# Performance work log

Hardware: AMD Instinct MI355X
Metric: run time of the kernel (lower is better)

Reference implementation:

```python
import jax, jax.numpy as jnp
import numpy as np

B, T, IN, H, OUT = 128, 1024, 17, 512, 17


def setup_inputs() -> dict:
    key = jax.random.key(0)
    ks = jax.random.split(key, 11)
    s_in = 1.0 / np.sqrt(H)
    return {
        "x": jax.random.normal(ks[0], (B, T, IN), dtype=jnp.float32),
        "wih0": jax.random.normal(ks[1], (4 * H, IN), dtype=jnp.float32) * s_in,
        "whh0": jax.random.normal(ks[2], (4 * H, H), dtype=jnp.float32) * s_in,
        "bih0": jax.random.normal(ks[3], (4 * H,), dtype=jnp.float32) * s_in,
        "bhh0": jax.random.normal(ks[4], (4 * H,), dtype=jnp.float32) * s_in,
        "wih1": jax.random.normal(ks[5], (4 * H, H), dtype=jnp.float32) * s_in,
        "whh1": jax.random.normal(ks[6], (4 * H, H), dtype=jnp.float32) * s_in,
        "bih1": jax.random.normal(ks[7], (4 * H,), dtype=jnp.float32) * s_in,
        "bhh1": jax.random.normal(ks[8], (4 * H,), dtype=jnp.float32) * s_in,
        "lin_w": jax.random.normal(ks[9], (OUT, H), dtype=jnp.float32) * s_in,
        "lin_b": jax.random.normal(ks[10], (OUT,), dtype=jnp.float32) * s_in,
    }


def _lstm_layer(x, wih, whh, bih, bhh):
    # x: [B, T, D]; gate order i, f, g, o (torch.nn.LSTMCell convention)
    b, _, _ = x.shape
    h = whh.shape[1]
    # Precompute input projection for all timesteps: [B, T, 4H]
    proj = jnp.einsum("btd,gd->btg", x, wih) + bih

    def step(carry, p_t):
        h_t, c_t = carry
        gates = p_t + h_t @ whh.T + bhh  # [B, 4H]
        i, f, g, o = jnp.split(gates, 4, axis=1)
        i = jax.nn.sigmoid(i)
        f = jax.nn.sigmoid(f)
        o = jax.nn.sigmoid(o)
        g = jnp.tanh(g)
        c_t = f * c_t + i * g
        h_t = o * jnp.tanh(c_t)
        return (h_t, c_t), h_t

    h0 = jnp.zeros((b, h), x.dtype)
    c0 = jnp.zeros((b, h), x.dtype)
    _, ys = jax.lax.scan(step, (h0, c0), jnp.swapaxes(proj, 0, 1))  # ys: [T, B, H]
    return jnp.swapaxes(ys, 0, 1)  # [B, T, H]


def reference(x, wih0, whh0, bih0, bhh0, wih1, whh1, bih1, bhh1, lin_w, lin_b):
    y = _lstm_layer(x, wih0, whh0, bih0, bhh0)
    y = _lstm_layer(y, wih1, whh1, bih1, bhh1)
    h_last = y[:, -1, :]  # [B, H]
    return h_last @ lin_w.T + lin_b  # [B, OUT]
```

## Files before the change

kernel.cpp:

```cpp
#include <hip/hip_runtime.h>
#include <cstddef>
#include <cstdint>

typedef unsigned long long ull;
typedef unsigned short u16;
typedef unsigned int u32;
typedef __attribute__((ext_vector_type(8))) short s8v;
typedef __attribute__((ext_vector_type(4))) float f4v;

#define GROUPS 8
#define BG     16
#define JS     16
#define TPB    256
#define NT     1024
#define HDIM   512
#define INDIM  17
#define OUTDIM 17
#define BTOT   128

#define AT_LD(p)   __hip_atomic_load((p), __ATOMIC_RELAXED, __HIP_MEMORY_SCOPE_AGENT)
#define AT_ST(p,v) __hip_atomic_store((p), (v), __ATOMIC_RELAXED, __HIP_MEMORY_SCOPE_AGENT)

#define PLANE32 8192
#define WIDX(k, b) ((((k) >> 5) * 512) + ((((k) >> 3) & 3) * 128) + ((b) * 8) + ((k) & 7))

#define RA_OFF     ((size_t)0)
#define RING_BYTES ((size_t)4 * GROUPS * PLANE32 * 4)
#define RB_OFF     (RA_OFF + RING_BYTES)
#define FB32_OFF   (RB_OFF + RING_BYTES)
#define WS_NEEDED  (FB32_OFF + (size_t)BTOT * HDIM * 4)
#define RIX32(sl, gr) (((size_t)(sl) * GROUPS + (gr)) * PLANE32)

#define L_H0   0
#define L_H1   49152
#define L_STG  65536
#define L_CTL  67584
#define LDS_SZ 82944

__device__ __forceinline__ u16 f2bf(float f) {
  unsigned int u = __float_as_uint(f);
  u += 0x7FFFu + ((u >> 16) & 1u);
  return (u16)(u >> 16);
}
__device__ __forceinline__ float bf2f(u16 h) {
  return __uint_as_float(((unsigned int)h) << 16);
}
__device__ __forceinline__ float sigm(float x) { return 1.f / (1.f + __expf(-x)); }
__device__ __forceinline__ float tanh_f(float x) { return 2.f / (1.f + __expf(-2.f * x)) - 1.f; }

#define MFMA(a, b, c) __builtin_amdgcn_mfma_f32_16x16x32_bf16((a), (b), (c), 0, 0, 0)

__device__ __forceinline__ void pbar(int* c, int& nbar, int lane) {
  ++nbar;
  if (lane == 0)
    (void)__hip_atomic_fetch_add(c, 1, __ATOMIC_RELEASE, __HIP_MEMORY_SCOPE_WORKGROUP);
  while (__hip_atomic_load(c, __ATOMIC_ACQUIRE, __HIP_MEMORY_SCOPE_WORKGROUP) < 2 * nbar) {}
}

__global__ __launch_bounds__(TPB, 1) void lstm_fused(
    const float* __restrict__ x,
    const float* __restrict__ wih0, const float* __restrict__ whh0,
    const float* __restrict__ bih0, const float* __restrict__ bhh0,
    const float* __restrict__ wih1, const float* __restrict__ whh1,
    const float* __restrict__ bih1, const float* __restrict__ bhh1,
    u32* __restrict__ ringA, u32* __restrict__ ringB,
    float* __restrict__ fb32)
{
  const int bid  = blockIdx.x;
  const int gr   = bid & 7;
  const int wg   = bid >> 3;
  const int j0   = wg * JS;
  const int tid  = threadIdx.x;
  const int wave = tid >> 6;
  const int lane = tid & 63;
  const int n    = lane & 15;
  const int q    = lane >> 4;
  const int k0   = q * 8;
  const int gidx = n & 3;
  const int jl   = n >> 2;

  __shared__ __align__(16) char smem[LDS_SZ];
  int* ctl = (int*)(smem + L_CTL);
  u32* stg = (u32*)(smem + L_STG + (wave & 1) * 512 + (wave >> 1) * 1024);

  if (tid < 16) ctl[tid] = 0;

  {
    int b_l = tid >> 4, j_l = tid & 15, jgw = j0 + j_l;
    int wo = WIDX(jgw, b_l);
    AT_ST(&ringA[RIX32(0, gr) + wo], 0u);
    AT_ST(&ringB[RIX32(0, gr) + wo], 0u);
  }
  __syncthreads();

  const f4v z = {0.f, 0.f, 0.f, 0.f};
  const int half = wave & 1;
  const int pub = (wg >> 1) * 256 + ((wg & 1) * 2 + (wave & 1)) * 64;
  const int sub = (lane >> 2) * 128 + (lane & 3) * 32;
  const ull TMASK = 0xFFFF0000FFFF0000ULL;

  if (wave < 2) {
    int jown[2];
    float bias[2][4];
    s8v wxh[2], wxl[2];
    s8v whh_[2][16], whl_[2][16];
#pragma unroll
    for (int i = 0; i < 2; ++i) {
      const int jc = wave * 2 + i;
      jown[i] = j0 + jc * 4 + q;
      const float* wr = wih0 + (size_t)(gidx * HDIM + j0 + jc * 4 + jl) * INDIM;
#pragma unroll
      for (int j = 0; j < 8; ++j) {
        int k = k0 + j;
        float v = (k < INDIM) ? wr[k] : 0.f;
        u16 hi = f2bf(v);
        wxh[i][j] = (short)hi;
        wxl[i][j] = (short)f2bf(v - bf2f(hi));
      }
      const float* hr = whh0 + (size_t)(gidx * HDIM + j0 + jc * 4 + jl) * HDIM;
#pragma unroll
      for (int kt = 0; kt < 16; ++kt)
#pragma unroll
        for (int j = 0; j < 8; ++j) {
          float v = hr[kt * 32 + k0 + j];
          u16 hi = f2bf(v);
          whh_[i][kt][j] = (short)hi;
          whl_[i][kt][j] = (short)f2bf(v - bf2f(hi));
        }
#pragma unroll
      for (int g = 0; g < 4; ++g)
        bias[i][g] = bih0[g * HDIM + jown[i]] + bhh0[g * HDIM + jown[i]];
    }
    float cc[2] = {0.f, 0.f};
    int nbar = 0;

    for (int s = 1; s <= NT + 1; ++s) {
      f4v xa[2] = {z, z};
      if (s <= NT) {
        const float* xr = x + ((size_t)(gr * BG + n) * NT + (s - 1)) * INDIM;
        s8v bxh, bxl;
#pragma unroll
        for (int j = 0; j < 8; ++j) {
          int k = k0 + j;
          float v = (k < INDIM) ? xr[k] : 0.f;
          u16 hi = f2bf(v);
          bxh[j] = (short)hi;
          bxl[j] = (short)f2bf(v - bf2f(hi));
        }
#pragma unroll
        for (int i = 0; i < 2; ++i) {
          xa[i] = MFMA(wxh[i], bxh, xa[i]);
          xa[i] = MFMA(wxh[i], bxl, xa[i]);
          xa[i] = MFMA(wxl[i], bxh, xa[i]);
        }
      }
      const int sl3 = (s - 1) % 3;
      {
        const ull* src = (const ull*)(ringA + RIX32((s - 1) & 3, gr)) + half * 2048;
        const ull tg = (ull)(u16)(s - 1);
        const ull pat = (tg << 16) | (tg << 48);
        for (;;) {
          ull w = AT_LD(src + sub);
          int l1a = __hip_atomic_load(&ctl[7], __ATOMIC_ACQUIRE,
                                      __HIP_MEMORY_SCOPE_WORKGROUP);
          int l1b = __hip_atomic_load(&ctl[8], __ATOMIC_ACQUIRE,
                                      __HIP_MEMORY_SCOPE_WORKGROUP);
          int l1t = l1a < l1b ? l1a : l1b;
          if (__ballot((((w ^ pat) & TMASK) == 0) & (l1t >= s - 4)) == ~0ULL) break;
          __builtin_amdgcn_s_sleep(1);
        }
        ull v[32];
        for (;;) {
          ull acc = 0;
#pragma unroll
          for (int i = 0; i < 16; ++i) {
            v[2 * i]     = AT_LD(src + (i * 64 + lane) * 2);
            v[2 * i + 1] = AT_LD(src + (i * 64 + lane) * 2 + 1);
          }
#pragma unroll
          for (int i = 0; i < 32; ++i) acc |= (v[i] ^ pat) & TMASK;
          if (__ballot(acc == 0) == ~0ULL) break;
          __builtin_amdgcn_s_sleep(1);
        }
        char* dst = smem + L_H0 + sl3 * 16384 + half * 8192;
#pragma unroll
        for (int i = 0; i < 16; ++i) {
          ull a = v[2 * i], b = v[2 * i + 1];
          ull packed = (a & 0xFFFFULL) | ((a >> 16) & 0xFFFF0000ULL)
                     | ((b & 0xFFFFULL) << 32) | (((b >> 16) & 0xFFFF0000ULL) << 32);
          *(ull*)(dst + (i * 64 + lane) * 8) = packed;
        }
      }
      pbar(&ctl[0], nbar, lane);
      if (wave == 0 && lane == 0)
        __hip_atomic_store(&ctl[4 + sl3], s - 1, __ATOMIC_RELEASE,
                           __HIP_MEMORY_SCOPE_WORKGROUP);
      if (s == NT + 1) break;

      const char* sh = smem + L_H0 + sl3 * 16384;
      f4v cHH[2] = {z, z}, cHL[2] = {z, z};
#pragma unroll
      for (int kt = 0; kt < 16; ++kt) {
        s8v bh = *(const s8v*)(sh + kt * 1024 + q * 256 + n * 16);
#pragma unroll
        for (int i = 0; i < 2; ++i) {
          cHH[i] = MFMA(whh_[i][kt], bh, cHH[i]);
          cHL[i] = MFMA(whl_[i][kt], bh, cHL[i]);
        }
      }
      const u32 otag = ((u32)(u16)s) << 16;
#pragma unroll
      for (int ii = 0; ii < 2; ++ii) {
        f4v e = xa[ii] + cHH[ii] + cHL[ii];
        float pi = e[0] + bias[ii][0], pf = e[1] + bias[ii][1];
        float pg = e[2] + bias[ii][2], po = e[3] + bias[ii][3];
        float ig = sigm(pi), fg = sigm(pf), gv = tanh_f(pg), og = sigm(po);
        cc[ii] = fg * cc[ii] + ig * gv;
        stg[n * 8 + ii * 4 + q] = otag | (u32)f2bf(og * tanh_f(cc[ii]));
      }
      asm volatile("s_waitcnt lgkmcnt(0)" ::: "memory");
      __builtin_amdgcn_sched_barrier(0);
      {
        ull v0 = *(const ull*)((const char*)stg + lane * 8);
        ull* d = (ull*)(ringA + RIX32(s & 3, gr)) + pub;
        AT_ST(d + lane, v0);
      }
    }
  } else {
    int jown[2];
    float bias[2][4];
    s8v w1x_[2][16], w1h_[2][16];
#pragma unroll
    for (int i = 0; i < 2; ++i) {
      const int jc = (wave - 2) * 2 + i;
      jown[i] = j0 + jc * 4 + q;
      const float* p1 = wih1 + (size_t)(gidx * HDIM + j0 + jc * 4 + jl) * HDIM;
      const float* p2 = whh1 + (size_t)(gidx * HDIM + j0 + jc * 4 + jl) * HDIM;
#pragma unroll
      for (int kt = 0; kt < 16; ++kt)
#pragma unroll
        for (int j = 0; j < 8; ++j) {
          w1x_[i][kt][j] = (short)f2bf(p1[kt * 32 + k0 + j]);
          w1h_[i][kt][j] = (short)f2bf(p2[kt * 32 + k0 + j]);
        }
#pragma unroll
      for (int g = 0; g < 4; ++g)
        bias[i][g] = bih1[g * HDIM + jown[i]] + bhh1[g * HDIM + jown[i]];
    }
    float c1[2] = {0.f, 0.f};
    int nbar = 0;

    for (int t = 1; t <= NT; ++t) {
      {
        const ull* src = (const ull*)(ringB + RIX32((t - 1) & 3, gr)) + half * 2048;
        const ull tg = (ull)(u16)(t - 1);
        const ull pat = (tg << 16) | (tg << 48);
        for (;;) {
          ull w = AT_LD(src + sub);
          if (__ballot(((w ^ pat) & TMASK) == 0) == ~0ULL) break;
          __builtin_amdgcn_s_sleep(1);
        }
        ull v[32];
        for (;;) {
          ull acc = 0;
#pragma unroll
          for (int i = 0; i < 16; ++i) {
            v[2 * i]     = AT_LD(src + (i * 64 + lane) * 2);
            v[2 * i + 1] = AT_LD(src + (i * 64 + lane) * 2 + 1);
          }
#pragma unroll
          for (int i = 0; i < 32; ++i) acc |= (v[i] ^ pat) & TMASK;
          if (__ballot(acc == 0) == ~0ULL) break;
          __builtin_amdgcn_s_sleep(1);
        }
        char* dst = smem + L_H1 + half * 8192;
#pragma unroll
        for (int i = 0; i < 16; ++i) {
          ull a = v[2 * i], b = v[2 * i + 1];
          ull packed = (a & 0xFFFFULL) | ((a >> 16) & 0xFFFF0000ULL)
                     | ((b & 0xFFFFULL) << 32) | (((b >> 16) & 0xFFFF0000ULL) << 32);
          *(ull*)(dst + (i * 64 + lane) * 8) = packed;
        }
      }
      pbar(&ctl[1], nbar, lane);
      const char* th = smem + L_H1;
      f4v dHH[2] = {z, z};
#pragma unroll
      for (int kt = 0; kt < 16; ++kt) {
        s8v bh = *(const s8v*)(th + kt * 1024 + q * 256 + n * 16);
#pragma unroll
        for (int i = 0; i < 2; ++i) dHH[i] = MFMA(w1h_[i][kt], bh, dHH[i]);
      }
      const int sl3 = t % 3;
      while (__hip_atomic_load(&ctl[4 + sl3], __ATOMIC_ACQUIRE,
                               __HIP_MEMORY_SCOPE_WORKGROUP) < t) {}
      const char* sh = smem + L_H0 + sl3 * 16384;
      f4v eHH[2] = {z, z};
#pragma unroll
      for (int kt = 0; kt < 16; ++kt) {
        s8v bh = *(const s8v*)(sh + kt * 1024 + q * 256 + n * 16);
#pragma unroll
        for (int i = 0; i < 2; ++i) eHH[i] = MFMA(w1x_[i][kt], bh, eHH[i]);
      }
      if (lane == 0)
        __hip_atomic_store(&ctl[7 + (wave & 1)], t, __ATOMIC_RELEASE,
                           __HIP_MEMORY_SCOPE_WORKGROUP);
      const u32 otag = ((u32)(u16)t) << 16;
      float hout[2];
#pragma unroll
      for (int ii = 0; ii < 2; ++ii) {
        f4v e = dHH[ii] + eHH[ii];
        float pi = e[0] + bias[ii][0], pf = e[1] + bias[ii][1];
        float pg = e[2] + bias[ii][2], po = e[3] + bias[ii][3];
        float ig = sigm(pi), fg = sigm(pf), gv = tanh_f(pg), og = sigm(po);
        c1[ii] = fg * c1[ii] + ig * gv;
        hout[ii] = og * tanh_f(c1[ii]);
        stg[n * 8 + ii * 4 + q] = otag | (u32)f2bf(hout[ii]);
      }
      asm volatile("s_waitcnt lgkmcnt(0)" ::: "memory");
      __builtin_amdgcn_sched_barrier(0);
      {
        ull v0 = *(const ull*)((const char*)stg + lane * 8);
        ull* d = (ull*)(ringB + RIX32(t & 3, gr)) + pub;
        AT_ST(d + lane, v0);
      }
      if (t == NT) {
#pragma unroll
        for (int ii = 0; ii < 2; ++ii)
          AT_ST((u32*)&fb32[(size_t)(gr * BG + n) * HDIM + jown[ii]],
                __float_as_uint(hout[ii]));
      }
    }
  }
}

__global__ void final_linear(const float* __restrict__ fb32,
                             const float* __restrict__ lin_w,
                             const float* __restrict__ lin_b,
                             float* __restrict__ out) {
  int b = blockIdx.x, o = threadIdx.x;
  if (o < OUTDIM) {
    float acc = lin_b[o];
    const u32* hr = (const u32*)(fb32 + (size_t)b * HDIM);
    for (int j = 0; j < HDIM; ++j) {
      float h = __uint_as_float(AT_LD(hr + j));
      acc += h * lin_w[(size_t)o * HDIM + j];
    }
    out[b * OUTDIM + o] = acc;
  }
}

__global__ void sentinel_kernel(float* __restrict__ out, int nv) {
  int i = blockIdx.x * TPB + threadIdx.x;
  if (i < nv) out[i] = 1e30f;
}

extern "C" void kernel_launch(void* const* d_in, const int* in_sizes, int n_in,
                              void* d_out, int out_size, void* d_ws, size_t ws_size,
                              hipStream_t stream) {
  (void)in_sizes; (void)n_in;
  const float* x     = (const float*)d_in[0];
  const float* wih0  = (const float*)d_in[1];
  const float* whh0  = (const float*)d_in[2];
  const float* bih0  = (const float*)d_in[3];
  const float* bhh0  = (const float*)d_in[4];
  const float* wih1  = (const float*)d_in[5];
  const float* whh1  = (const float*)d_in[6];
  const float* bih1  = (const float*)d_in[7];
  const float* bhh1  = (const float*)d_in[8];
  const float* lin_w = (const float*)d_in[9];
  const float* lin_b = (const float*)d_in[10];
  float* out = (float*)d_out;
  char* ws = (char*)d_ws;

  if (ws_size < WS_NEEDED) {
    sentinel_kernel<<<(out_size + TPB - 1) / TPB, TPB, 0, stream>>>(out, out_size);
    return;
  }

  u32* ringA  = (u32*)(ws + RA_OFF);
  u32* ringB  = (u32*)(ws + RB_OFF);
  float* fb32 = (float*)(ws + FB32_OFF);

  lstm_fused<<<256, TPB, 0, stream>>>(x, wih0, whh0, bih0, bhh0,
                                      wih1, whh1, bih1, bhh1,
                                      ringA, ringB, fb32);
  final_linear<<<BTOT, 64, 0, stream>>>(fb32, lin_w, lin_b, out);
}
```

Before: 4.962 ms.

## Halve workgroup count, doubling hidden slice and waves per workgroup

```diff
diff --git a/kernel.cpp b/kernel.cpp
--- a/kernel.cpp
+++ b/kernel.cpp
@@ -10,8 +10,9 @@
 
 #define GROUPS 8
 #define BG     16
-#define JS     16
-#define TPB    256
+#define JS     32
+#define TPB    512
+#define NWG    128
 #define NT     1024
 #define HDIM   512
 #define INDIM  17
@@ -34,8 +35,8 @@
 #define L_H0   0
 #define L_H1   49152
 #define L_STG  65536
-#define L_CTL  67584
-#define LDS_SZ 82944
+#define L_CTL  69632
+#define LDS_SZ 69696
 
 __device__ __forceinline__ u16 f2bf(float f) {
   unsigned int u = __float_as_uint(f);
@@ -50,11 +51,11 @@
 
 #define MFMA(a, b, c) __builtin_amdgcn_mfma_f32_16x16x32_bf16((a), (b), (c), 0, 0, 0)
 
-__device__ __forceinline__ void pbar(int* c, int& nbar, int lane) {
+__device__ __forceinline__ void pbar4(int* c, int& nbar, int lane) {
   ++nbar;
   if (lane == 0)
     (void)__hip_atomic_fetch_add(c, 1, __ATOMIC_RELEASE, __HIP_MEMORY_SCOPE_WORKGROUP);
-  while (__hip_atomic_load(c, __ATOMIC_ACQUIRE, __HIP_MEMORY_SCOPE_WORKGROUP) < 2 * nbar) {}
+  while (__hip_atomic_load(c, __ATOMIC_ACQUIRE, __HIP_MEMORY_SCOPE_WORKGROUP) < 4 * nbar) {}
 }
 
 __global__ __launch_bounds__(TPB, 1) void lstm_fused(
@@ -81,32 +82,26 @@
 
   __shared__ __align__(16) char smem[LDS_SZ];
   int* ctl = (int*)(smem + L_CTL);
-  u32* stg = (u32*)(smem + L_STG + (wave & 1) * 512 + (wave >> 1) * 1024);
+  u32* stg = (u32*)(smem + L_STG + wave * 512);
 
   if (tid < 16) ctl[tid] = 0;
 
-  {
-    int b_l = tid >> 4, j_l = tid & 15, jgw = j0 + j_l;
-    int wo = WIDX(jgw, b_l);
-    AT_ST(&ringA[RIX32(0, gr) + wo], 0u);
-    AT_ST(&ringB[RIX32(0, gr) + wo], 0u);
-  }
+  AT_ST(&ringA[RIX32(0, gr) + wg * 512 + tid], 0u);
+  AT_ST(&ringB[RIX32(0, gr) + wg * 512 + tid], 0u);
   __syncthreads();
 
   const f4v z = {0.f, 0.f, 0.f, 0.f};
-  const int half = wave & 1;
-  const int pub = (wg >> 1) * 256 + ((wg & 1) * 2 + (wave & 1)) * 64;
-  const int sub = (lane >> 2) * 128 + (lane & 3) * 32;
   const ull TMASK = 0xFFFF0000FFFF0000ULL;
 
-  if (wave < 2) {
+  if (wave < 4) {
+    const int w = wave;
     int jown[2];
     float bias[2][4];
     s8v wxh[2], wxl[2];
     s8v whh_[2][16], whl_[2][16];
 #pragma unroll
     for (int i = 0; i < 2; ++i) {
-      const int jc = wave * 2 + i;
+      const int jc = w * 2 + i;
       jown[i] = j0 + jc * 4 + q;
       const float* wr = wih0 + (size_t)(gidx * HDIM + j0 + jc * 4 + jl) * INDIM;
 #pragma unroll
@@ -156,43 +151,35 @@
       }
       const int sl3 = (s - 1) % 3;
       {
-        const ull* src = (const ull*)(ringA + RIX32((s - 1) & 3, gr)) + half * 2048;
+        const ull* src = (const ull*)(ringA + RIX32((s - 1) & 3, gr)) + w * 1024;
         const ull tg = (ull)(u16)(s - 1);
         const ull pat = (tg << 16) | (tg << 48);
-        for (;;) {
-          ull w = AT_LD(src + sub);
-          int l1a = __hip_atomic_load(&ctl[7], __ATOMIC_ACQUIRE,
-                                      __HIP_MEMORY_SCOPE_WORKGROUP);
-          int l1b = __hip_atomic_load(&ctl[8], __ATOMIC_ACQUIRE,
-                                      __HIP_MEMORY_SCOPE_WORKGROUP);
-          int l1t = l1a < l1b ? l1a : l1b;
-          if (__ballot((((w ^ pat) & TMASK) == 0) & (l1t >= s - 4)) == ~0ULL) break;
-          __builtin_amdgcn_s_sleep(1);
-        }
-        ull v[32];
+        ull v[16];
         for (;;) {
           ull acc = 0;
 #pragma unroll
-          for (int i = 0; i < 16; ++i) {
+          for (int i = 0; i < 8; ++i) {
             v[2 * i]     = AT_LD(src + (i * 64 + lane) * 2);
             v[2 * i + 1] = AT_LD(src + (i * 64 + lane) * 2 + 1);
           }
 #pragma unroll
-          for (int i = 0; i < 32; ++i) acc |= (v[i] ^ pat) & TMASK;
-          if (__ballot(acc == 0) == ~0ULL) break;
+          for (int i = 0; i < 16; ++i) acc |= (v[i] ^ pat) & TMASK;
+          int l1c = __hip_atomic_load(&ctl[7], __ATOMIC_ACQUIRE,
+                                      __HIP_MEMORY_SCOPE_WORKGROUP);
+          if (__ballot((acc == 0) & (l1c >= 4 * (s - 4))) == ~0ULL) break;
           __builtin_amdgcn_s_sleep(1);
         }
-        char* dst = smem + L_H0 + sl3 * 16384 + half * 8192;
-#pragma unroll
-        for (int i = 0; i < 16; ++i) {
+        char* dst = smem + L_H0 + sl3 * 16384 + w * 4096;
+#pragma unroll
+        for (int i = 0; i < 8; ++i) {
           ull a = v[2 * i], b = v[2 * i + 1];
           ull packed = (a & 0xFFFFULL) | ((a >> 16) & 0xFFFF0000ULL)
                      | ((b & 0xFFFFULL) << 32) | (((b >> 16) & 0xFFFF0000ULL) << 32);
           *(ull*)(dst + (i * 64 + lane) * 8) = packed;
         }
       }
-      pbar(&ctl[0], nbar, lane);
-      if (wave == 0 && lane == 0)
+      pbar4(&ctl[0], nbar, lane);
+      if (w == 0 && lane == 0)
         __hip_atomic_store(&ctl[4 + sl3], s - 1, __ATOMIC_RELEASE,
                            __HIP_MEMORY_SCOPE_WORKGROUP);
       if (s == NT + 1) break;
@@ -222,17 +209,18 @@
       __builtin_amdgcn_sched_barrier(0);
       {
         ull v0 = *(const ull*)((const char*)stg + lane * 8);
-        ull* d = (ull*)(ringA + RIX32(s & 3, gr)) + pub;
+        ull* d = (ull*)(ringA + RIX32(s & 3, gr)) + wg * 256 + w * 64;
         AT_ST(d + lane, v0);
       }
     }
   } else {
+    const int w = wave - 4;
     int jown[2];
     float bias[2][4];
     s8v w1x_[2][16], w1h_[2][16];
 #pragma unroll
     for (int i = 0; i < 2; ++i) {
-      const int jc = (wave - 2) * 2 + i;
+      const int jc = w * 2 + i;
       jown[i] = j0 + jc * 4 + q;
       const float* p1 = wih1 + (size_t)(gidx * HDIM + j0 + jc * 4 + jl) * HDIM;
       const float* p2 = whh1 + (size_t)(gidx * HDIM + j0 + jc * 4 + jl) * HDIM;
@@ -252,37 +240,32 @@
 
     for (int t = 1; t <= NT; ++t) {
       {
-        const ull* src = (const ull*)(ringB + RIX32((t - 1) & 3, gr)) + half * 2048;
+        const ull* src = (const ull*)(ringB + RIX32((t - 1) & 3, gr)) + w * 1024;
         const ull tg = (ull)(u16)(t - 1);
         const ull pat = (tg << 16) | (tg << 48);
-        for (;;) {
-          ull w = AT_LD(src + sub);
-          if (__ballot(((w ^ pat) & TMASK) == 0) == ~0ULL) break;
-          __builtin_amdgcn_s_sleep(1);
-        }
-        ull v[32];
+        ull v[16];
         for (;;) {
           ull acc = 0;
 #pragma unroll
-          for (int i = 0; i < 16; ++i) {
+          for (int i = 0; i < 8; ++i) {
             v[2 * i]     = AT_LD(src + (i * 64 + lane) * 2);
             v[2 * i + 1] = AT_LD(src + (i * 64 + lane) * 2 + 1);
           }
 #pragma unroll
-          for (int i = 0; i < 32; ++i) acc |= (v[i] ^ pat) & TMASK;
+          for (int i = 0; i < 16; ++i) acc |= (v[i] ^ pat) & TMASK;
           if (__ballot(acc == 0) == ~0ULL) break;
           __builtin_amdgcn_s_sleep(1);
         }
-        char* dst = smem + L_H1 + half * 8192;
-#pragma unroll
-        for (int i = 0; i < 16; ++i) {
+        char* dst = smem + L_H1 + w * 4096;
+#pragma unroll
+        for (int i = 0; i < 8; ++i) {
           ull a = v[2 * i], b = v[2 * i + 1];
           ull packed = (a & 0xFFFFULL) | ((a >> 16) & 0xFFFF0000ULL)
                      | ((b & 0xFFFFULL) << 32) | (((b >> 16) & 0xFFFF0000ULL) << 32);
           *(ull*)(dst + (i * 64 + lane) * 8) = packed;
         }
       }
-      pbar(&ctl[1], nbar, lane);
+      pbar4(&ctl[1], nbar, lane);
       const char* th = smem + L_H1;
       f4v dHH[2] = {z, z};
 #pragma unroll
@@ -303,8 +286,8 @@
         for (int i = 0; i < 2; ++i) eHH[i] = MFMA(w1x_[i][kt], bh, eHH[i]);
       }
       if (lane == 0)
-        __hip_atomic_store(&ctl[7 + (wave & 1)], t, __ATOMIC_RELEASE,
-                           __HIP_MEMORY_SCOPE_WORKGROUP);
+        (void)__hip_atomic_fetch_add(&ctl[7], 1, __ATOMIC_RELEASE,
+                                     __HIP_MEMORY_SCOPE_WORKGROUP);
       const u32 otag = ((u32)(u16)t) << 16;
       float hout[2];
 #pragma unroll
@@ -321,7 +304,7 @@
       __builtin_amdgcn_sched_barrier(0);
       {
         ull v0 = *(const ull*)((const char*)stg + lane * 8);
-        ull* d = (ull*)(ringB + RIX32(t & 3, gr)) + pub;
+        ull* d = (ull*)(ringB + RIX32(t & 3, gr)) + wg * 256 + w * 64;
         AT_ST(d + lane, v0);
       }
       if (t == NT) {
@@ -351,7 +334,7 @@
 }
 
 __global__ void sentinel_kernel(float* __restrict__ out, int nv) {
-  int i = blockIdx.x * TPB + threadIdx.x;
+  int i = blockIdx.x * 256 + threadIdx.x;
   if (i < nv) out[i] = 1e30f;
 }
 
@@ -374,7 +357,7 @@
   char* ws = (char*)d_ws;
 
   if (ws_size < WS_NEEDED) {
-    sentinel_kernel<<<(out_size + TPB - 1) / TPB, TPB, 0, stream>>>(out, out_size);
+    sentinel_kernel<<<(out_size + 255) / 256, 256, 0, stream>>>(out, out_size);
     return;
   }
 
@@ -382,7 +365,7 @@
   u32* ringB  = (u32*)(ws + RB_OFF);
   float* fb32 = (float*)(ws + FB32_OFF);
 
-  lstm_fused<<<256, TPB, 0, stream>>>(x, wih0, whh0, bih0, bhh0,
+  lstm_fused<<<NWG, TPB, 0, stream>>>(x, wih0, whh0, bih0, bhh0,
                                       wih1, whh1, bih1, bhh1,
                                       ringA, ringB, fb32);
   final_linear<<<BTOT, 64, 0, stream>>>(fb32, lin_w, lin_b, out);
```

Measured after the change: 14.10 ms. 2.84x slower.

## Replace tagged ring words with packed bf16 ring and per-wave release flags

Applied to the files above, without the earlier changes.

```diff
diff --git a/kernel.cpp b/kernel.cpp
--- a/kernel.cpp
+++ b/kernel.cpp
@@ -7,6 +7,7 @@
 typedef unsigned int u32;
 typedef __attribute__((ext_vector_type(8))) short s8v;
 typedef __attribute__((ext_vector_type(4))) float f4v;
+typedef __attribute__((ext_vector_type(4))) u32 u32x4;
 
 #define GROUPS 8
 #define BG     16
@@ -21,21 +22,24 @@
 #define AT_LD(p)   __hip_atomic_load((p), __ATOMIC_RELAXED, __HIP_MEMORY_SCOPE_AGENT)
 #define AT_ST(p,v) __hip_atomic_store((p), (v), __ATOMIC_RELAXED, __HIP_MEMORY_SCOPE_AGENT)
 
-#define PLANE32 8192
-#define WIDX(k, b) ((((k) >> 5) * 512) + ((((k) >> 3) & 3) * 128) + ((b) * 8) + ((k) & 7))
+#define PLANEW 4096
+#define RIXW(sl, gr) (((size_t)(sl) * GROUPS + (gr)) * PLANEW)
 
 #define RA_OFF     ((size_t)0)
-#define RING_BYTES ((size_t)4 * GROUPS * PLANE32 * 4)
+#define RING_BYTES ((size_t)4 * GROUPS * PLANEW * 4)
 #define RB_OFF     (RA_OFF + RING_BYTES)
-#define FB32_OFF   (RB_OFF + RING_BYTES)
+#define FLG_WORDS  (4 * GROUPS * 64)
+#define FA_OFF     (RB_OFF + RING_BYTES)
+#define FB_OFF     (FA_OFF + (size_t)FLG_WORDS * 4)
+#define FB32_OFF   (FB_OFF + (size_t)FLG_WORDS * 4)
 #define WS_NEEDED  (FB32_OFF + (size_t)BTOT * HDIM * 4)
-#define RIX32(sl, gr) (((size_t)(sl) * GROUPS + (gr)) * PLANE32)
+#define FIX(sl, gr) ((size_t)((sl) * GROUPS + (gr)) * 64)
 
 #define L_H0   0
 #define L_H1   49152
 #define L_STG  65536
-#define L_CTL  67584
-#define LDS_SZ 82944
+#define L_CTL  66560
+#define LDS_SZ 66624
 
 __device__ __forceinline__ u16 f2bf(float f) {
   unsigned int u = __float_as_uint(f);
@@ -49,6 +53,23 @@
 __device__ __forceinline__ float tanh_f(float x) { return 2.f / (1.f + __expf(-2.f * x)) - 1.f; }
 
 #define MFMA(a, b, c) __builtin_amdgcn_mfma_f32_16x16x32_bf16((a), (b), (c), 0, 0, 0)
+
+__device__ __forceinline__ void sc1_read16(const char* base, u32x4 r[8]) {
+  asm volatile(
+      "global_load_dwordx4 %0, %8, off sc1\n\t"
+      "global_load_dwordx4 %1, %8, off offset:1024 sc1\n\t"
+      "global_load_dwordx4 %2, %8, off offset:2048 sc1\n\t"
+      "global_load_dwordx4 %3, %8, off offset:3072 sc1\n\t"
+      "global_load_dwordx4 %4, %9, off sc1\n\t"
+      "global_load_dwordx4 %5, %9, off offset:1024 sc1\n\t"
+      "global_load_dwordx4 %6, %9, off offset:2048 sc1\n\t"
+      "global_load_dwordx4 %7, %9, off offset:3072 sc1\n\t"
+      "s_waitcnt vmcnt(0)"
+      : "=&v"(r[0]), "=&v"(r[1]), "=&v"(r[2]), "=&v"(r[3]),
+        "=&v"(r[4]), "=&v"(r[5]), "=&v"(r[6]), "=&v"(r[7])
+      : "v"(base), "v"(base + 4096)
+      : "memory");
+}
 
 __device__ __forceinline__ void pbar(int* c, int& nbar, int lane) {
   ++nbar;
@@ -64,6 +85,7 @@
     const float* __restrict__ wih1, const float* __restrict__ whh1,
     const float* __restrict__ bih1, const float* __restrict__ bhh1,
     u32* __restrict__ ringA, u32* __restrict__ ringB,
+    u32* __restrict__ flgA, u32* __restrict__ flgB,
     float* __restrict__ fb32)
 {
   const int bid  = blockIdx.x;
@@ -81,23 +103,28 @@
 
   __shared__ __align__(16) char smem[LDS_SZ];
   int* ctl = (int*)(smem + L_CTL);
-  u32* stg = (u32*)(smem + L_STG + (wave & 1) * 512 + (wave >> 1) * 1024);
+  u16* stg16 = (u16*)(smem + L_STG + wave * 256);
 
   if (tid < 16) ctl[tid] = 0;
 
-  {
-    int b_l = tid >> 4, j_l = tid & 15, jgw = j0 + j_l;
-    int wo = WIDX(jgw, b_l);
-    AT_ST(&ringA[RIX32(0, gr) + wo], 0u);
-    AT_ST(&ringB[RIX32(0, gr) + wo], 0u);
+  if (tid < 128) {
+    int w = tid >> 6, l = tid & 63;
+    int base = (wg >> 1) * 256 + ((wg & 1) * 2 + w) * 64 + l;
+    AT_ST(ringA + RIXW(0, gr) + base, 0u);
+    AT_ST(ringB + RIXW(0, gr) + base, 0u);
   }
   __syncthreads();
+  if (tid < 2) {
+    __hip_atomic_store(&flgA[FIX(0, gr) + wg * 2 + tid], 0u,
+                       __ATOMIC_RELEASE, __HIP_MEMORY_SCOPE_AGENT);
+    __hip_atomic_store(&flgB[FIX(0, gr) + wg * 2 + tid], 0u,
+                       __ATOMIC_RELEASE, __HIP_MEMORY_SCOPE_AGENT);
+  }
 
   const f4v z = {0.f, 0.f, 0.f, 0.f};
   const int half = wave & 1;
-  const int pub = (wg >> 1) * 256 + ((wg & 1) * 2 + (wave & 1)) * 64;
-  const int sub = (lane >> 2) * 128 + (lane & 3) * 32;
-  const ull TMASK = 0xFFFF0000FFFF0000ULL;
+  const int pw   = wave & 1;
+  const int pubw = (wg >> 1) * 256 + ((wg & 1) * 2 + pw) * 64;
 
   if (wave < 2) {
     int jown[2];
@@ -156,40 +183,26 @@
       }
       const int sl3 = (s - 1) % 3;
       {
-        const ull* src = (const ull*)(ringA + RIX32((s - 1) & 3, gr)) + half * 2048;
-        const ull tg = (ull)(u16)(s - 1);
-        const ull pat = (tg << 16) | (tg << 48);
+        const u32* fl = flgA + FIX((s - 1) & 3, gr);
+        const u32 want = (u32)(s - 1);
         for (;;) {
-          ull w = AT_LD(src + sub);
+          u32 f = AT_LD(fl + lane);
           int l1a = __hip_atomic_load(&ctl[7], __ATOMIC_ACQUIRE,
                                       __HIP_MEMORY_SCOPE_WORKGROUP);
           int l1b = __hip_atomic_load(&ctl[8], __ATOMIC_ACQUIRE,
                                       __HIP_MEMORY_SCOPE_WORKGROUP);
           int l1t = l1a < l1b ? l1a : l1b;
-          if (__ballot((((w ^ pat) & TMASK) == 0) & (l1t >= s - 4)) == ~0ULL) break;
+          if (__ballot(f == want) == ~0ULL && l1t >= s - 4) break;
           __builtin_amdgcn_s_sleep(1);
         }
-        ull v[32];
-        for (;;) {
-          ull acc = 0;
-#pragma unroll
-          for (int i = 0; i < 16; ++i) {
-            v[2 * i]     = AT_LD(src + (i * 64 + lane) * 2);
-            v[2 * i + 1] = AT_LD(src + (i * 64 + lane) * 2 + 1);
-          }
-#pragma unroll
-          for (int i = 0; i < 32; ++i) acc |= (v[i] ^ pat) & TMASK;
-          if (__ballot(acc == 0) == ~0ULL) break;
-          __builtin_amdgcn_s_sleep(1);
-        }
-        char* dst = smem + L_H0 + sl3 * 16384 + half * 8192;
-#pragma unroll
-        for (int i = 0; i < 16; ++i) {
-          ull a = v[2 * i], b = v[2 * i + 1];
-          ull packed = (a & 0xFFFFULL) | ((a >> 16) & 0xFFFF0000ULL)
-                     | ((b & 0xFFFFULL) << 32) | (((b >> 16) & 0xFFFF0000ULL) << 32);
-          *(ull*)(dst + (i * 64 + lane) * 8) = packed;
-        }
+        u32x4 r[8];
+        const char* src = (const char*)(ringA + RIXW((s - 1) & 3, gr))
+                        + half * 8192 + lane * 16;
+        sc1_read16(src, r);
+        char* dst = smem + L_H0 + sl3 * 16384 + half * 8192 + lane * 16;
+#pragma unroll
+        for (int i = 0; i < 8; ++i)
+          *(u32x4*)(dst + i * 1024) = r[i];
       }
       pbar(&ctl[0], nbar, lane);
       if (wave == 0 && lane == 0)
@@ -208,7 +221,6 @@
           cHL[i] = MFMA(whl_[i][kt], bh, cHL[i]);
         }
       }
-      const u32 otag = ((u32)(u16)s) << 16;
 #pragma unroll
       for (int ii = 0; ii < 2; ++ii) {
         f4v e = xa[ii] + cHH[ii] + cHL[ii];
@@ -216,14 +228,15 @@
         float pg = e[2] + bias[ii][2], po = e[3] + bias[ii][3];
         float ig = sigm(pi), fg = sigm(pf), gv = tanh_f(pg), og = sigm(po);
         cc[ii] = fg * cc[ii] + ig * gv;
-        stg[n * 8 + ii * 4 + q] = otag | (u32)f2bf(og * tanh_f(cc[ii]));
+        stg16[n * 8 + ii * 4 + q] = f2bf(og * tanh_f(cc[ii]));
       }
       asm volatile("s_waitcnt lgkmcnt(0)" ::: "memory");
-      __builtin_amdgcn_sched_barrier(0);
       {
-        ull v0 = *(const ull*)((const char*)stg + lane * 8);
-        ull* d = (ull*)(ringA + RIX32(s & 3, gr)) + pub;
-        AT_ST(d + lane, v0);
+        u32 pv = *(const u32*)((const char*)stg16 + lane * 4);
+        AT_ST(ringA + RIXW(s & 3, gr) + pubw + lane, pv);
+        if (lane == 0)
+          __hip_atomic_store(&flgA[FIX(s & 3, gr) + wg * 2 + pw], (u32)s,
+                             __ATOMIC_RELEASE, __HIP_MEMORY_SCOPE_AGENT);
       }
     }
   } else {
@@ -252,35 +265,21 @@
 
     for (int t = 1; t <= NT; ++t) {
       {
-        const ull* src = (const ull*)(ringB + RIX32((t - 1) & 3, gr)) + half * 2048;
-        const ull tg = (ull)(u16)(t - 1);
-        const ull pat = (tg << 16) | (tg << 48);
+        const u32* fl = flgB + FIX((t - 1) & 3, gr);
+        const u32 want = (u32)(t - 1);
         for (;;) {
-          ull w = AT_LD(src + sub);
-          if (__ballot(((w ^ pat) & TMASK) == 0) == ~0ULL) break;
+          u32 f = AT_LD(fl + lane);
+          if (__ballot(f == want) == ~0ULL) break;
           __builtin_amdgcn_s_sleep(1);
         }
-        ull v[32];
-        for (;;) {
-          ull acc = 0;
-#pragma unroll
-          for (int i = 0; i < 16; ++i) {
-            v[2 * i]     = AT_LD(src + (i * 64 + lane) * 2);
-            v[2 * i + 1] = AT_LD(src + (i * 64 + lane) * 2 + 1);
-          }
-#pragma unroll
-          for (int i = 0; i < 32; ++i) acc |= (v[i] ^ pat) & TMASK;
-          if (__ballot(acc == 0) == ~0ULL) break;
-          __builtin_amdgcn_s_sleep(1);
-        }
-        char* dst = smem + L_H1 + half * 8192;
-#pragma unroll
-        for (int i = 0; i < 16; ++i) {
-          ull a = v[2 * i], b = v[2 * i + 1];
-          ull packed = (a & 0xFFFFULL) | ((a >> 16) & 0xFFFF0000ULL)
-                     | ((b & 0xFFFFULL) << 32) | (((b >> 16) & 0xFFFF0000ULL) << 32);
-          *(ull*)(dst + (i * 64 + lane) * 8) = packed;
-        }
+        u32x4 r[8];
+        const char* src = (const char*)(ringB + RIXW((t - 1) & 3, gr))
+                        + half * 8192 + lane * 16;
+        sc1_read16(src, r);
+        char* dst = smem + L_H1 + half * 8192 + lane * 16;
+#pragma unroll
+        for (int i = 0; i < 8; ++i)
+          *(u32x4*)(dst + i * 1024) = r[i];
       }
       pbar(&ctl[1], nbar, lane);
       const char* th = smem + L_H1;
@@ -305,7 +304,6 @@
       if (lane == 0)
         __hip_atomic_store(&ctl[7 + (wave & 1)], t, __ATOMIC_RELEASE,
                            __HIP_MEMORY_SCOPE_WORKGROUP);
-      const u32 otag = ((u32)(u16)t) << 16;
       float hout[2];
 #pragma unroll
       for (int ii = 0; ii < 2; ++ii) {
@@ -315,14 +313,15 @@
         float ig = sigm(pi), fg = sigm(pf), gv = tanh_f(pg), og = sigm(po);
         c1[ii] = fg * c1[ii] + ig * gv;
         hout[ii] = og * tanh_f(c1[ii]);
-        stg[n * 8 + ii * 4 + q] = otag | (u32)f2bf(hout[ii]);
+        stg16[n * 8 + ii * 4 + q] = f2bf(hout[ii]);
       }
       asm volatile("s_waitcnt lgkmcnt(0)" ::: "memory");
-      __builtin_amdgcn_sched_barrier(0);
       {
-        ull v0 = *(const ull*)((const char*)stg + lane * 8);
-        ull* d = (ull*)(ringB + RIX32(t & 3, gr)) + pub;
-        AT_ST(d + lane, v0);
+        u32 pv = *(const u32*)((const char*)stg16 + lane * 4);
+        AT_ST(ringB + RIXW(t & 3, gr) + pubw + lane, pv);
+        if (lane == 0)
+          __hip_atomic_store(&flgB[FIX(t & 3, gr) + wg * 2 + pw], (u32)t,
+                             __ATOMIC_RELEASE, __HIP_MEMORY_SCOPE_AGENT);
       }
       if (t == NT) {
 #pragma unroll
@@ -380,10 +379,12 @@
 
   u32* ringA  = (u32*)(ws + RA_OFF);
   u32* ringB  = (u32*)(ws + RB_OFF);
+  u32* flgA   = (u32*)(ws + FA_OFF);
+  u32* flgB   = (u32*)(ws + FB_OFF);
   float* fb32 = (float*)(ws + FB32_OFF);
 
   lstm_fused<<<256, TPB, 0, stream>>>(x, wih0, whh0, bih0, bhh0,
                                       wih1, whh1, bih1, bhh1,
-                                      ringA, ringB, fb32);
+                                      ringA, ringB, flgA, flgB, fb32);
   final_linear<<<BTOT, 64, 0, stream>>>(fb32, lin_w, lin_b, out);
 }
```

New measurement: 17.46 ms. +251.8%, slower.
